# Kernel tuning notes

Hardware: AMD Instinct MI355X
Metric: run time of the kernel (lower is better)

## Reference

```python
import jax, jax.numpy as jnp
import numpy as np

C_A = 768; C_S = 384; C_Z = 128; H = 16; D = C_A // H
B = 1; N = 4096; NQ = 32; NK = 128; NB = N // NQ
EPS = 1e-5


def _ln(x):
    # layernorm without learned affine (affine applied by caller where present)
    m = jnp.mean(x, axis=-1, keepdims=True)
    v = jnp.mean((x - m) ** 2, axis=-1, keepdims=True)
    return (x - m) * jax.lax.rsqrt(v + EPS)


def setup_inputs() -> dict:
    key = jax.random.key(0)
    ks = jax.random.split(key, 16)
    w = lambda k, shp: jax.random.normal(k, shp, dtype=jnp.float32) * 0.02
    return dict(
        a=jax.random.normal(ks[0], (B, N, C_A), jnp.float32),
        s=jax.random.normal(ks[1], (B, N, C_S), jnp.float32),
        z=jax.random.normal(ks[2], (B, NB, NQ, NK, C_Z), jnp.float32),
        adaln_gamma_s=jnp.ones((C_S,), jnp.float32),
        adaln_ws=w(ks[3], (C_S, C_A)),
        adaln_bs=jnp.zeros((C_A,), jnp.float32),
        adaln_wskip=w(ks[4], (C_S, C_A)),
        lnz_gamma=jnp.ones((C_Z,), jnp.float32),
        wz=w(ks[5], (C_Z, H)),
        wq=w(ks[6], (C_A, C_A)), bq=jnp.zeros((C_A,), jnp.float32),
        wk=w(ks[7], (C_A, C_A)),
        wv=w(ks[8], (C_A, C_A)),
        wg=w(ks[9], (C_A, C_A)), bg=jnp.ones((C_A,), jnp.float32),
        wo=w(ks[10], (C_A, C_A)), bo=jnp.zeros((C_A,), jnp.float32),
        w_last=w(ks[11], (C_S, C_A)),
        b_last=jnp.full((C_A,), -2.0, jnp.float32),  # biasinit = -2.0
        n_queries=NQ, n_keys=NK,
    )


def _forward(a, s, z, adaln_gamma_s, adaln_ws, adaln_bs, adaln_wskip,
             lnz_gamma, wz, wq, bq, wk, wv, wg, bg, wo, bo,
             w_last, b_last, n_queries, n_keys):
    Bq, Nq, _ = a.shape
    nb = Nq // n_queries
    # AdaptiveLayerNorm (AF3 Alg 26): a <- sigmoid(Lin(s_ln)) * LN(a) + LinNoBias(s_ln)
    s_ln = _ln(s) * adaln_gamma_s
    a_ln = jax.nn.sigmoid(s_ln @ adaln_ws + adaln_bs) * _ln(a) + s_ln @ adaln_wskip
    # pair bias: LN(z) (no offset) -> per-head bias, permuted to [B,H,nb,nq,nk]
    bias = (_ln(z) * lnz_gamma) @ wz                    # [B, nb, nq, nk, H]
    bias = jnp.transpose(bias, (0, 4, 1, 2, 3))          # [B, H, nb, nq, nk]
    # projections (q has bias; k/v no bias)
    q = (a_ln @ wq + bq).reshape(Bq, nb, n_queries, H, D)
    k = (a_ln @ wk).reshape(Bq, Nq, H, D)
    v = (a_ln @ wv).reshape(Bq, Nq, H, D)
    # local window: query block w covers [w*nq, (w+1)*nq); keys are nk centered on it
    start = jnp.arange(nb) * n_queries + n_queries // 2 - n_keys // 2
    kidx = start[:, None] + jnp.arange(n_keys)[None, :]  # [nb, nk]
    valid = (kidx >= 0) & (kidx < Nq)
    kidx = jnp.clip(kidx, 0, Nq - 1)
    k_loc = k[:, kidx]                                    # [B, nb, nk, H, D]
    v_loc = v[:, kidx]
    scale = 1.0 / float(np.sqrt(D))
    scores = jnp.einsum('bwqhd,bwkhd->bhwqk', q, k_loc) * scale + bias
    scores = jnp.where(valid[None, None, :, None, :], scores, -1e9)
    p = jax.nn.softmax(scores, axis=-1)
    o = jnp.einsum('bhwqk,bwkhd->bwqhd', p, v_loc).reshape(Bq, Nq, C_A)
    # gating, output projection, final sigmoid gate from raw s
    o = (jax.nn.sigmoid(a_ln @ wg + bg) * o) @ wo + bo
    return jax.nn.sigmoid(s @ w_last + b_last) * o


def reference(a, s, z, adaln_gamma_s, adaln_ws, adaln_bs, adaln_wskip,
              lnz_gamma, wz, wq, bq, wk, wv, wg, bg, wo, bo,
              w_last, b_last, n_queries, n_keys):
    return _forward(a, s, z, adaln_gamma_s, adaln_ws, adaln_bs, adaln_wskip,
                    lnz_gamma, wz, wq, bq, wk, wv, wg, bg, wo, bo,
                    w_last, b_last, n_queries, n_keys)
```

## Files before the change

### kernel.cpp

```cpp
#include <hip/hip_runtime.h>
#include <hip/hip_bf16.h>
#include <math.h>

#define N_TOK 4096
#define CA 768
#define CS 384
#define CZ 128
#define NHEAD 16
#define DH 48
#define NQW 32
#define NKW 128
#define NBLK 128
#define VT_W 4224

typedef __attribute__((ext_vector_type(8))) short short8;
typedef __attribute__((ext_vector_type(4))) float float4v;
typedef __attribute__((ext_vector_type(4))) unsigned short ushort4v;

__device__ __forceinline__ float sigmoidf_(float x){ return 1.0f/(1.0f+__expf(-x)); }

__device__ __forceinline__ unsigned short f2bf(float x){
  unsigned u = __float_as_uint(x);
  unsigned r = (u + 0x7FFFu + ((u>>16)&1u)) >> 16;
  return (unsigned short)r;
}
__device__ __forceinline__ float bf2f(unsigned short b){
  return __uint_as_float(((unsigned)b)<<16);
}
__device__ __forceinline__ short8 cvt8(const float* xv){
  union { short8 v; unsigned short u[8]; } H;
  #pragma unroll
  for (int j=0;j<8;j++) H.u[j] = f2bf(xv[j]);
  return H.v;
}

__device__ __forceinline__ void gload_lds16(const void* gsrc, void* ldst){
  __builtin_amdgcn_global_load_lds(
    (const __attribute__((address_space(1))) void*)gsrc,
    (__attribute__((address_space(3))) void*)ldst, 16, 0, 0);
}

__global__ __launch_bounds__(256) void prep_kernel(
  const float* __restrict__ s, const float* __restrict__ adaln_gamma,
  unsigned short* __restrict__ s_ln_h, unsigned short* __restrict__ s_h,
  const float* __restrict__ a, float* __restrict__ a_n,
  const float* __restrict__ ws, const float* __restrict__ wskip,
  const float* __restrict__ wq, const float* __restrict__ wk,
  const float* __restrict__ wv, const float* __restrict__ wg,
  const float* __restrict__ wo, const float* __restrict__ wlast,
  unsigned short* __restrict__ Wt1, unsigned short* __restrict__ Wt2,
  unsigned short* __restrict__ Wt3, unsigned short* __restrict__ Wt4,
  const float* __restrict__ bq, const float* __restrict__ bg,
  float* __restrict__ biasq)
{
  __shared__ float tile[64][65];
  int bid = blockIdx.x;
  int tid = threadIdx.x;

  if (bid < 1024){
    int wave = tid>>6, lane = tid&63;
    int row = bid*4 + wave;
    const float* x = s + (size_t)row*CS;
    float v[6]; float sum=0.f, sq=0.f;
    #pragma unroll
    for (int i=0;i<6;i++){ v[i]=x[lane+64*i]; sum+=v[i]; sq+=v[i]*v[i]; }
    #pragma unroll
    for (int off=32; off; off>>=1){ sum+=__shfl_xor(sum,off); sq+=__shfl_xor(sq,off); }
    float m = sum*(1.f/CS);
    float var = sq*(1.f/CS)-m*m;
    float rs = rsqrtf(var+1e-5f);
    #pragma unroll
    for (int i=0;i<6;i++){
      int c = lane+64*i;
      s_ln_h[(size_t)row*CS+c] = f2bf((v[i]-m)*rs*adaln_gamma[c]);
      s_h[(size_t)row*CS+c]    = f2bf(v[i]);
    }
    return;
  }
  bid -= 1024;

  if (bid < 1024){
    int wave = tid>>6, lane = tid&63;
    int row = bid*4 + wave;
    const float* x = a + (size_t)row*CA;
    float v[12]; float sum=0.f, sq=0.f;
    #pragma unroll
    for (int i=0;i<12;i++){ v[i]=x[lane+64*i]; sum+=v[i]; sq+=v[i]*v[i]; }
    #pragma unroll
    for (int off=32; off; off>>=1){ sum+=__shfl_xor(sum,off); sq+=__shfl_xor(sq,off); }
    float m = sum*(1.f/CA);
    float var = sq*(1.f/CA)-m*m;
    float rs = rsqrtf(var+1e-5f);
    float* o = a_n + (size_t)row*CA;
    #pragma unroll
    for (int i=0;i<12;i++) o[lane+64*i] = (v[i]-m)*rs;
    return;
  }
  bid -= 1024;

  if (bid < 936){
    const float* src; unsigned short* dst; int K; int local;
    if      (bid < 72)  { src=ws;    dst=Wt1;                   K=CS; local=bid; }
    else if (bid < 144) { src=wskip; dst=Wt1 + (size_t)768*CS;  K=CS; local=bid-72; }
    else if (bid < 288) { src=wq;    dst=Wt2;                   K=CA; local=bid-144; }
    else if (bid < 432) { src=wk;    dst=Wt2 + (size_t)768*CA;  K=CA; local=bid-288; }
    else if (bid < 576) { src=wv;    dst=Wt2 + (size_t)1536*CA; K=CA; local=bid-432; }
    else if (bid < 720) { src=wg;    dst=Wt2 + (size_t)2304*CA; K=CA; local=bid-576; }
    else if (bid < 864) { src=wo;    dst=Wt3;                   K=CA; local=bid-720; }
    else                { src=wlast; dst=Wt4;                   K=CS; local=bid-864; }
    int ktiles = K/64;
    int kb = (local % ktiles)*64, nb = (local / ktiles)*64;
    int c = tid & 63, r0 = tid >> 6;
    #pragma unroll
    for (int i=0;i<16;i++){
      int r = r0 + 4*i;
      tile[r][c] = src[(size_t)(kb+r)*CA + nb + c];
    }
    __syncthreads();
    #pragma unroll
    for (int i=0;i<16;i++){
      int r = r0 + 4*i;
      dst[(size_t)(nb+r)*K + kb + c] = f2bf(tile[c][r]);
    }
    return;
  }
  bid -= 936;

  int i = bid*256 + tid;
  float v = 0.f;
  if (i < 768) v = bq[i];
  else if (i >= 2304) v = bg[i-2304];
  biasq[i] = v;
}

__global__ __launch_bounds__(256) void zbias_kernel(const float* __restrict__ z,
                                                    const float* __restrict__ gamma,
                                                    const float* __restrict__ wz,
                                                    unsigned short* __restrict__ bias3){
  __shared__ float tbuf[4][16*132];
  int tid = threadIdx.x, wave = tid>>6, lane = tid&63;
  int lr = lane&15, quad = lane>>4;

  short8 bwh[4];
  float w1 = 0.f;
  #pragma unroll
  for (int ks=0;ks<4;ks++){
    float wv[8];
    #pragma unroll
    for (int j=0;j<8;j++){
      int k = ks*32 + quad*8 + j;
      wv[j] = wz[k*NHEAD + lr]*gamma[k];
      w1 += wv[j];
    }
    bwh[ks] = cvt8(wv);
  }
  w1 += __shfl_xor(w1, 16);
  w1 += __shfl_xor(w1, 32);

  size_t group = (size_t)blockIdx.x*4 + wave;
  const float* zg = z + group*(size_t)(NKW*CZ);

  float4 bufA[8], bufB[8];
  auto loadrow = [&](int b, float4* dst){
    const float* zr = zg + (size_t)(b*16 + lr)*CZ + quad*8;
    #pragma unroll
    for (int ks=0;ks<4;ks++){
      dst[ks*2]   = *(const float4*)(zr + ks*32);
      dst[ks*2+1] = *(const float4*)(zr + ks*32 + 4);
    }
  };
  auto process = [&](int b, const float4* d){
    float sum=0.f, sq=0.f;
    #pragma unroll
    for (int p=0;p<8;p++){
      sum += d[p].x + d[p].y + d[p].z + d[p].w;
      sq  += d[p].x*d[p].x + d[p].y*d[p].y + d[p].z*d[p].z + d[p].w*d[p].w;
    }
    sum += __shfl_xor(sum,16); sum += __shfl_xor(sum,32);
    sq  += __shfl_xor(sq,16);  sq  += __shfl_xor(sq,32);
    float mean = sum*(1.f/CZ);
    float var = sq*(1.f/CZ) - mean*mean;
    float rs = rsqrtf(var + 1e-5f);

    float4v c = (float4v){0.f,0.f,0.f,0.f};
    #pragma unroll
    for (int ks=0;ks<4;ks++){
      float xv[8];
      xv[0]=d[ks*2].x;   xv[1]=d[ks*2].y;   xv[2]=d[ks*2].z;   xv[3]=d[ks*2].w;
      xv[4]=d[ks*2+1].x; xv[5]=d[ks*2+1].y; xv[6]=d[ks*2+1].z; xv[7]=d[ks*2+1].w;
      c = __builtin_amdgcn_mfma_f32_16x16x32_bf16(cvt8(xv), bwh[ks], c, 0,0,0);
    }
    #pragma unroll
    for (int r=0;r<4;r++){
      int rrow = quad*4 + r;
      float m_r  = __shfl(mean, rrow);
      float rs_r = __shfl(rs, rrow);
      tbuf[wave][lr*132 + b*16 + rrow] = rs_r*(c[r] - m_r*w1);
    }
  };

  loadrow(0, bufA);
  #pragma unroll 1
  for (int bb=0;bb<4;bb++){
    loadrow(bb*2+1, bufB);
    process(bb*2, bufA);
    if (bb<3) loadrow(bb*2+2, bufA);
    process(bb*2+1, bufB);
  }

  #pragma unroll
  for (int i=0;i<8;i++){
    int h = i*2 + (lane>>5);
    int koff = (lane&31)*4;
    float4 vv = *(const float4*)&tbuf[wave][h*132 + koff];
    ushort4v o4 = { f2bf(vv.x), f2bf(vv.y), f2bf(vv.z), f2bf(vv.w) };
    *(ushort4v*)(bias3 + group*2048 + h*128 + koff) = o4;
  }
}

__global__ __launch_bounds__(256) void adaln_gemm(
  const unsigned short* __restrict__ A, const unsigned short* __restrict__ Bt,
  const float* __restrict__ bs, const float* __restrict__ a_n,
  unsigned short* __restrict__ outh)
{
  __shared__ unsigned short Ash[128*32];
  __shared__ unsigned short B1sh[128*32];
  __shared__ unsigned short B2sh[128*32];

  int tid = threadIdx.x;
  int w = tid >> 6, lane = tid & 63;
  int lr = lane & 15, quad = lane >> 4;
  int m0 = blockIdx.y*128, n0 = blockIdx.x*128;
  int mbase = (w&1)*64, nbase = (w>>1)*64;

  float4v acc1[4][4], acc2[4][4];
  #pragma unroll
  for (int i=0;i<4;i++)
    #pragma unroll
    for (int j=0;j<4;j++){
      acc1[i][j] = (float4v){0.f,0.f,0.f,0.f};
      acc2[i][j] = (float4v){0.f,0.f,0.f,0.f};
    }

  int grow = w*32 + (lane>>2);
  int gcol8 = (lane&3)*8;

  for (int k0=0; k0<CS; k0+=32){
    __syncthreads();
    #pragma unroll
    for (int i=0;i<2;i++){
      int rA = grow + i*16;
      gload_lds16(A  + (size_t)(m0 + rA)*CS + k0 + gcol8, &Ash[(w*32 + i*16)*32]);
      gload_lds16(Bt + (size_t)(n0 + rA)*CS + k0 + gcol8, &B1sh[(w*32 + i*16)*32]);
      gload_lds16(Bt + (size_t)(768 + n0 + rA)*CS + k0 + gcol8, &B2sh[(w*32 + i*16)*32]);
    }
    __syncthreads();

    short8 af[4], b1f[4], b2f[4];
    #pragma unroll
    for (int mi=0;mi<4;mi++)
      af[mi] = *(const short8*)&Ash[(mbase + mi*16 + lr)*32 + quad*8];
    #pragma unroll
    for (int ni=0;ni<4;ni++){
      b1f[ni] = *(const short8*)&B1sh[(nbase + ni*16 + lr)*32 + quad*8];
      b2f[ni] = *(const short8*)&B2sh[(nbase + ni*16 + lr)*32 + quad*8];
    }
    #pragma unroll
    for (int mi=0;mi<4;mi++)
      #pragma unroll
      for (int ni=0;ni<4;ni++){
        acc1[mi][ni] = __builtin_amdgcn_mfma_f32_16x16x32_bf16(af[mi], b1f[ni], acc1[mi][ni], 0,0,0);
        acc2[mi][ni] = __builtin_amdgcn_mfma_f32_16x16x32_bf16(af[mi], b2f[ni], acc2[mi][ni], 0,0,0);
      }
  }

  #pragma unroll
  for (int ni=0;ni<4;ni++){
    int col = n0 + nbase + ni*16 + lr;
    float bsv = bs[col];
    #pragma unroll
    for (int mi=0;mi<4;mi++){
      #pragma unroll
      for (int reg=0;reg<4;reg++){
        int row = m0 + mbase + mi*16 + quad*4 + reg;
        float v = sigmoidf_(acc1[mi][ni][reg] + bsv)*a_n[(size_t)row*CA + col] + acc2[mi][ni][reg];
        outh[(size_t)row*CA + col] = f2bf(v);
      }
    }
  }
}

template<int MODE>
__global__ __launch_bounds__(256) void gemm_bf16(
  const unsigned short* __restrict__ A1, const unsigned short* __restrict__ B1,
  const float* __restrict__ bias1, int K1,
  const unsigned short* __restrict__ A2, const unsigned short* __restrict__ B2,
  const float* __restrict__ bias2, int K2,
  void* __restrict__ outp, int M, int N)
{
  __shared__ unsigned short Ash[128*32];
  __shared__ unsigned short Bsh[128*32];

  int tid = threadIdx.x;
  int w = tid >> 6, lane = tid & 63;
  int lr = lane & 15, quad = lane >> 4;
  int m0 = blockIdx.y*128, n0 = blockIdx.x*128;
  int mbase = (w&1)*64, nbase = (w>>1)*64;

  float4v acc1[4][4];
  float4v acc2[4][4];
  #pragma unroll
  for (int i=0;i<4;i++)
    #pragma unroll
    for (int j=0;j<4;j++){
      acc1[i][j] = (float4v){0.f,0.f,0.f,0.f};
      if constexpr (MODE == 3) acc2[i][j] = (float4v){0.f,0.f,0.f,0.f};
    }

  int grow = w*32 + (lane>>2);
  int gcol8 = (lane&3)*8;

  for (int k0=0; k0<K1; k0+=32){
    __syncthreads();
    #pragma unroll
    for (int i=0;i<2;i++){
      int rA = grow + i*16;
      gload_lds16(A1 + (size_t)(m0 + rA)*K1 + k0 + gcol8, &Ash[(w*32 + i*16)*32]);
      gload_lds16(B1 + (size_t)(n0 + rA)*K1 + k0 + gcol8, &Bsh[(w*32 + i*16)*32]);
    }
    __syncthreads();

    short8 af[4], bf[4];
    #pragma unroll
    for (int mi=0;mi<4;mi++)
      af[mi] = *(const short8*)&Ash[(mbase + mi*16 + lr)*32 + quad*8];
    #pragma unroll
    for (int ni=0;ni<4;ni++)
      bf[ni] = *(const short8*)&Bsh[(nbase + ni*16 + lr)*32 + quad*8];
    #pragma unroll
    for (int mi=0;mi<4;mi++)
      #pragma unroll
      for (int ni=0;ni<4;ni++)
        acc1[mi][ni] = __builtin_amdgcn_mfma_f32_16x16x32_bf16(af[mi], bf[ni], acc1[mi][ni], 0,0,0);
  }

  if constexpr (MODE == 3){
    for (int k0=0; k0<K2; k0+=32){
      __syncthreads();
      #pragma unroll
      for (int i=0;i<2;i++){
        int rA = grow + i*16;
        gload_lds16(A2 + (size_t)(m0 + rA)*K2 + k0 + gcol8, &Ash[(w*32 + i*16)*32]);
        gload_lds16(B2 + (size_t)(n0 + rA)*K2 + k0 + gcol8, &Bsh[(w*32 + i*16)*32]);
      }
      __syncthreads();

      short8 af[4], bf[4];
      #pragma unroll
      for (int mi=0;mi<4;mi++)
        af[mi] = *(const short8*)&Ash[(mbase + mi*16 + lr)*32 + quad*8];
      #pragma unroll
      for (int ni=0;ni<4;ni++)
        bf[ni] = *(const short8*)&Bsh[(nbase + ni*16 + lr)*32 + quad*8];
      #pragma unroll
      for (int mi=0;mi<4;mi++)
        #pragma unroll
        for (int ni=0;ni<4;ni++)
          acc2[mi][ni] = __builtin_amdgcn_mfma_f32_16x16x32_bf16(af[mi], bf[ni], acc2[mi][ni], 0,0,0);
    }
  }

  #pragma unroll
  for (int ni=0;ni<4;ni++){
    int col = n0 + nbase + ni*16 + lr;
    float bv1 = bias1 ? bias1[col] : 0.f;
    float bv2 = (MODE==3 && bias2) ? bias2[col] : 0.f;
    #pragma unroll
    for (int mi=0;mi<4;mi++){
      #pragma unroll
      for (int reg=0;reg<4;reg++){
        int row = m0 + mbase + mi*16 + quad*4 + reg;
        float x1 = acc1[mi][ni][reg] + bv1;
        if constexpr (MODE == 1)
          ((unsigned short*)outp)[(size_t)row*N + col] = f2bf(x1);
        else
          ((float*)outp)[(size_t)row*N + col] = sigmoidf_(acc2[mi][ni][reg] + bv2)*x1;
      }
    }
  }
}

__global__ __launch_bounds__(256) void vtrans_kernel(const unsigned short* __restrict__ qh,
                                                     unsigned short* __restrict__ Vt){
  __shared__ unsigned short tile[64][66];
  int t0 = blockIdx.x*64, c0 = blockIdx.y*64;
  int tid = threadIdx.x;
  int c = tid & 63, r0 = tid >> 6;
  #pragma unroll
  for (int i=0;i<16;i++){
    int r = r0 + 4*i;
    tile[r][c] = qh[(size_t)(t0+r)*3072 + 1536 + c0 + c];
  }
  if (t0 == 0){
    #pragma unroll
    for (int i=0;i<16;i++){
      int r = r0 + 4*i;
      Vt[(size_t)(c0+r)*VT_W + c] = 0;
    }
  } else if (t0 == N_TOK-64){
    #pragma unroll
    for (int i=0;i<16;i++){
      int r = r0 + 4*i;
      Vt[(size_t)(c0+r)*VT_W + 64 + N_TOK + c] = 0;
    }
  }
  __syncthreads();
  #pragma unroll
  for (int i=0;i<16;i++){
    int r = r0 + 4*i;
    Vt[(size_t)(c0+r)*VT_W + 64 + t0 + c] = tile[c][r];
  }
}

__global__ __launch_bounds__(256) void attn_kernel(
  const unsigned short* __restrict__ qh,
  const unsigned short* __restrict__ Vt,
  const unsigned short* __restrict__ bias3h,
  unsigned short* __restrict__ og)
{
  __shared__ unsigned short Pb[4][32*40];
  int tid = threadIdx.x, wave = tid>>6, lane = tid&63;
  int lr = lane&15, quad = lane>>4;
  int w = blockIdx.x, h = blockIdx.y*4 + wave;
  int start = w*NQW - 48;
  const float scale = 0.14433756729740643f;

  short8 zero8 = {0,0,0,0,0,0,0,0};

  short8 aq[2][2];
  #pragma unroll
  for (int mt=0;mt<2;mt++){
    int row = w*NQW + mt*16 + lr;
    const unsigned short* qp = qh + (size_t)row*3072 + h*DH;
    aq[mt][0] = *(const short8*)(qp + quad*8);
    aq[mt][1] = (quad<2) ? *(const short8*)(qp + 32 + quad*8) : zero8;
  }

  float4v c[2][8];
  #pragma unroll
  for (int mt=0;mt<2;mt++)
    #pragma unroll
    for (int nt=0;nt<8;nt++) c[mt][nt] = (float4v){0.f,0.f,0.f,0.f};

  #pragma unroll 1
  for (int nt=0;nt<8;nt++){
    int krc = min(max(start + nt*16 + lr,0),N_TOK-1);
    const unsigned short* kp = qh + (size_t)krc*3072 + 768 + h*DH;
    short8 bk0 = *(const short8*)(kp + quad*8);
    short8 bk1 = (quad<2) ? *(const short8*)(kp + 32 + quad*8) : zero8;
    #pragma unroll
    for (int mt=0;mt<2;mt++){
      c[mt][nt] = __builtin_amdgcn_mfma_f32_16x16x32_bf16(aq[mt][0], bk0, c[mt][nt], 0,0,0);
      c[mt][nt] = __builtin_amdgcn_mfma_f32_16x16x32_bf16(aq[mt][1], bk1, c[mt][nt], 0,0,0);
    }
  }

  float rmax[2][4], rsum[2][4];
  #pragma unroll
  for (int mt=0;mt<2;mt++)
    #pragma unroll
    for (int r=0;r<4;r++){ rmax[mt][r] = -3.0e38f; rsum[mt][r] = 0.f; }

  #pragma unroll
  for (int nt=0;nt<8;nt++){
    int key = start + nt*16 + lr;
    bool valid = (key>=0) && (key<N_TOK);
    #pragma unroll
    for (int mt=0;mt<2;mt++){
      #pragma unroll
      for (int r=0;r<4;r++){
        int q = mt*16 + quad*4 + r;
        float bv = bf2f(bias3h[(((size_t)(w*NQW+q))*NHEAD + h)*128 + nt*16 + lr]);
        float v = valid ? (c[mt][nt][r]*scale + bv) : -1e9f;
        c[mt][nt][r] = v;
        rmax[mt][r] = fmaxf(rmax[mt][r], v);
      }
    }
  }
  #pragma unroll
  for (int mt=0;mt<2;mt++)
    #pragma unroll
    for (int r=0;r<4;r++){
      float m = rmax[mt][r];
      m = fmaxf(m, __shfl_xor(m,1)); m = fmaxf(m, __shfl_xor(m,2));
      m = fmaxf(m, __shfl_xor(m,4)); m = fmaxf(m, __shfl_xor(m,8));
      rmax[mt][r] = m;
    }
  #pragma unroll
  for (int nt=0;nt<8;nt++)
    #pragma unroll
    for (int mt=0;mt<2;mt++)
      #pragma unroll
      for (int r=0;r<4;r++){
        float e = __expf(c[mt][nt][r] - rmax[mt][r]);
        c[mt][nt][r] = e;
        rsum[mt][r] += e;
      }
  #pragma unroll
  for (int mt=0;mt<2;mt++)
    #pragma unroll
    for (int r=0;r<4;r++){
      float sv = rsum[mt][r];
      sv += __shfl_xor(sv,1); sv += __shfl_xor(sv,2);
      sv += __shfl_xor(sv,4); sv += __shfl_xor(sv,8);
      rsum[mt][r] = 1.f/sv;
    }

  unsigned short* ph = &Pb[wave][0];
  float4v o[2][3];
  #pragma unroll
  for (int mt=0;mt<2;mt++)
    #pragma unroll
    for (int no=0;no<3;no++) o[mt][no] = (float4v){0.f,0.f,0.f,0.f};

  #pragma unroll 1
  for (int c2=0;c2<2;c2++){
    #pragma unroll 1
    for (int ks=0;ks<2;ks++){
      int ntb = c2*4 + ks*2;
      #pragma unroll
      for (int t=0;t<2;t++){
        int nt = ntb + t;
        #pragma unroll
        for (int mt=0;mt<2;mt++){
          #pragma unroll
          for (int r=0;r<4;r++){
            int q = mt*16 + quad*4 + r;
            ph[q*40 + t*16 + lr] = f2bf(c[mt][nt][r]*rsum[mt][r]);
          }
        }
      }
      short8 pa[2];
      #pragma unroll
      for (int mt=0;mt<2;mt++)
        pa[mt] = *(const short8*)&ph[(mt*16+lr)*40 + quad*8];
      #pragma unroll
      for (int no=0;no<3;no++){
        int col = h*DH + no*16 + lr;
        const unsigned short* vp = Vt + (size_t)col*VT_W + 64 + start + c2*64 + ks*32 + quad*8;
        short8 bv = *(const short8*)vp;
        #pragma unroll
        for (int mt=0;mt<2;mt++)
          o[mt][no] = __builtin_amdgcn_mfma_f32_16x16x32_bf16(pa[mt], bv, o[mt][no], 0,0,0);
      }
    }
  }

  #pragma unroll
  for (int mt=0;mt<2;mt++){
    #pragma unroll
    for (int no=0;no<3;no++){
      int d = no*16 + lr;
      #pragma unroll
      for (int r=0;r<4;r++){
        int q = mt*16 + quad*4 + r;
        size_t grow = (size_t)(w*NQW + q);
        float g = bf2f(qh[grow*3072 + 2304 + h*DH + d]);
        og[grow*CA + h*DH + d] = f2bf(o[mt][no][r] * sigmoidf_(g));
      }
    }
  }
}

extern "C" void kernel_launch(void* const* d_in, const int* in_sizes, int n_in,
                              void* d_out, int out_size, void* d_ws, size_t ws_size,
                              hipStream_t stream)
{
  const float* a            = (const float*)d_in[0];
  const float* s            = (const float*)d_in[1];
  const float* z            = (const float*)d_in[2];
  const float* adaln_gamma  = (const float*)d_in[3];
  const float* adaln_ws     = (const float*)d_in[4];
  const float* adaln_bs     = (const float*)d_in[5];
  const float* adaln_wskip  = (const float*)d_in[6];
  const float* lnz_gamma    = (const float*)d_in[7];
  const float* wz           = (const float*)d_in[8];
  const float* wq           = (const float*)d_in[9];
  const float* bq           = (const float*)d_in[10];
  const float* wk           = (const float*)d_in[11];
  const float* wv           = (const float*)d_in[12];
  const float* wg           = (const float*)d_in[13];
  const float* bg           = (const float*)d_in[14];
  const float* wo           = (const float*)d_in[15];
  const float* bo           = (const float*)d_in[16];
  const float* w_last       = (const float*)d_in[17];
  const float* b_last       = (const float*)d_in[18];
  float* out = (float*)d_out;

  char* base = (char*)d_ws;
  size_t off = 0;
  auto alloc = [&](size_t bytes)->char*{ char* p = base + off; off += (bytes + 255) & ~(size_t)255; return p; };

  unsigned short* s_ln_h = (unsigned short*)alloc((size_t)N_TOK*CS*2);
  unsigned short* s_h    = (unsigned short*)alloc((size_t)N_TOK*CS*2);
  float*          a_n    = (float*)alloc((size_t)N_TOK*CA*4);
  unsigned short* a_ln_h = (unsigned short*)alloc((size_t)N_TOK*CA*2);
  unsigned short* og_h   = (unsigned short*)alloc((size_t)N_TOK*CA*2);
  unsigned short* Wt1    = (unsigned short*)alloc((size_t)1536*CS*2);
  unsigned short* Wt2    = (unsigned short*)alloc((size_t)3072*CA*2);
  unsigned short* Wt3    = (unsigned short*)alloc((size_t)CA*CA*2);
  unsigned short* Wt4    = (unsigned short*)alloc((size_t)CA*CS*2);
  unsigned short* bias3h = (unsigned short*)alloc((size_t)N_TOK*NHEAD*NKW*2);
  unsigned short* qkvg_h = (unsigned short*)alloc((size_t)N_TOK*3072*2);
  unsigned short* Vt     = (unsigned short*)alloc((size_t)CA*VT_W*2);
  float*          biasq  = (float*)alloc((size_t)3072*4);

  prep_kernel<<<dim3(1024+1024+936+12), 256, 0, stream>>>(
      s, adaln_gamma, s_ln_h, s_h, a, a_n,
      adaln_ws, adaln_wskip, wq, wk, wv, wg, wo, w_last,
      Wt1, Wt2, Wt3, Wt4, bq, bg, biasq);

  zbias_kernel<<<dim3(N_TOK/4), 256, 0, stream>>>(z, lnz_gamma, wz, bias3h);

  adaln_gemm<<<dim3(CA/128, N_TOK/128), 256, 0, stream>>>(s_ln_h, Wt1, adaln_bs, a_n, a_ln_h);

  gemm_bf16<1><<<dim3(3072/128, N_TOK/128), 256, 0, stream>>>(
      a_ln_h, Wt2, biasq, CA, nullptr, nullptr, nullptr, 0, qkvg_h, N_TOK, 3072);

  vtrans_kernel<<<dim3(N_TOK/64, CA/64), 256, 0, stream>>>(qkvg_h, Vt);

  attn_kernel<<<dim3(NBLK, 4), 256, 0, stream>>>(qkvg_h, Vt, bias3h, og_h);

  gemm_bf16<3><<<dim3(CA/128, N_TOK/128), 256, 0, stream>>>(
      og_h, Wt3, bo, CA, s_h, Wt4, b_last, CS, out, N_TOK, CA);
}
```

Before: 234.8 us.

## Double-buffer GEMM tiles, fuse z-bias into QKVG GEMM launch, prefetch V in attention

All three GEMM kernels now double-buffer their LDS tiles so the global loads for the next K-step are issued before the current step's MFMAs, with one barrier per iteration instead of two. The z-bias layernorm/projection work is merged into the QKVG GEMM launch by interleaving block roles (3 GEMM blocks per 4 z-bias blocks), so the memory-bound z read can overlap compute-bound GEMM tiles. The final GEMM runs both K loops as one pipelined loop. The attention kernel gets launch bounds of 2, partial unrolling of the QK loop, and V fragments prefetched into registers ahead of the softmax, at the cost of more registers and possible spills.

New measurement: 278.0 us. 18.4% more time.

```diff
diff --git a/kernel.cpp b/kernel.cpp
--- a/kernel.cpp
+++ b/kernel.cpp
@@ -133,99 +133,14 @@
   biasq[i] = v;
 }
 
-__global__ __launch_bounds__(256) void zbias_kernel(const float* __restrict__ z,
-                                                    const float* __restrict__ gamma,
-                                                    const float* __restrict__ wz,
-                                                    unsigned short* __restrict__ bias3){
-  __shared__ float tbuf[4][16*132];
-  int tid = threadIdx.x, wave = tid>>6, lane = tid&63;
-  int lr = lane&15, quad = lane>>4;
-
-  short8 bwh[4];
-  float w1 = 0.f;
-  #pragma unroll
-  for (int ks=0;ks<4;ks++){
-    float wv[8];
-    #pragma unroll
-    for (int j=0;j<8;j++){
-      int k = ks*32 + quad*8 + j;
-      wv[j] = wz[k*NHEAD + lr]*gamma[k];
-      w1 += wv[j];
-    }
-    bwh[ks] = cvt8(wv);
-  }
-  w1 += __shfl_xor(w1, 16);
-  w1 += __shfl_xor(w1, 32);
-
-  size_t group = (size_t)blockIdx.x*4 + wave;
-  const float* zg = z + group*(size_t)(NKW*CZ);
-
-  float4 bufA[8], bufB[8];
-  auto loadrow = [&](int b, float4* dst){
-    const float* zr = zg + (size_t)(b*16 + lr)*CZ + quad*8;
-    #pragma unroll
-    for (int ks=0;ks<4;ks++){
-      dst[ks*2]   = *(const float4*)(zr + ks*32);
-      dst[ks*2+1] = *(const float4*)(zr + ks*32 + 4);
-    }
-  };
-  auto process = [&](int b, const float4* d){
-    float sum=0.f, sq=0.f;
-    #pragma unroll
-    for (int p=0;p<8;p++){
-      sum += d[p].x + d[p].y + d[p].z + d[p].w;
-      sq  += d[p].x*d[p].x + d[p].y*d[p].y + d[p].z*d[p].z + d[p].w*d[p].w;
-    }
-    sum += __shfl_xor(sum,16); sum += __shfl_xor(sum,32);
-    sq  += __shfl_xor(sq,16);  sq  += __shfl_xor(sq,32);
-    float mean = sum*(1.f/CZ);
-    float var = sq*(1.f/CZ) - mean*mean;
-    float rs = rsqrtf(var + 1e-5f);
-
-    float4v c = (float4v){0.f,0.f,0.f,0.f};
-    #pragma unroll
-    for (int ks=0;ks<4;ks++){
-      float xv[8];
-      xv[0]=d[ks*2].x;   xv[1]=d[ks*2].y;   xv[2]=d[ks*2].z;   xv[3]=d[ks*2].w;
-      xv[4]=d[ks*2+1].x; xv[5]=d[ks*2+1].y; xv[6]=d[ks*2+1].z; xv[7]=d[ks*2+1].w;
-      c = __builtin_amdgcn_mfma_f32_16x16x32_bf16(cvt8(xv), bwh[ks], c, 0,0,0);
-    }
-    #pragma unroll
-    for (int r=0;r<4;r++){
-      int rrow = quad*4 + r;
-      float m_r  = __shfl(mean, rrow);
-      float rs_r = __shfl(rs, rrow);
-      tbuf[wave][lr*132 + b*16 + rrow] = rs_r*(c[r] - m_r*w1);
-    }
-  };
-
-  loadrow(0, bufA);
-  #pragma unroll 1
-  for (int bb=0;bb<4;bb++){
-    loadrow(bb*2+1, bufB);
-    process(bb*2, bufA);
-    if (bb<3) loadrow(bb*2+2, bufA);
-    process(bb*2+1, bufB);
-  }
-
-  #pragma unroll
-  for (int i=0;i<8;i++){
-    int h = i*2 + (lane>>5);
-    int koff = (lane&31)*4;
-    float4 vv = *(const float4*)&tbuf[wave][h*132 + koff];
-    ushort4v o4 = { f2bf(vv.x), f2bf(vv.y), f2bf(vv.z), f2bf(vv.w) };
-    *(ushort4v*)(bias3 + group*2048 + h*128 + koff) = o4;
-  }
-}
-
 __global__ __launch_bounds__(256) void adaln_gemm(
   const unsigned short* __restrict__ A, const unsigned short* __restrict__ Bt,
   const float* __restrict__ bs, const float* __restrict__ a_n,
   unsigned short* __restrict__ outh)
 {
-  __shared__ unsigned short Ash[128*32];
-  __shared__ unsigned short B1sh[128*32];
-  __shared__ unsigned short B2sh[128*32];
+  __shared__ unsigned short Ash[2][128*32];
+  __shared__ unsigned short B1sh[2][128*32];
+  __shared__ unsigned short B2sh[2][128*32];
 
   int tid = threadIdx.x;
   int w = tid >> 6, lane = tid & 63;
@@ -245,25 +160,31 @@
   int grow = w*32 + (lane>>2);
   int gcol8 = (lane&3)*8;
 
-  for (int k0=0; k0<CS; k0+=32){
-    __syncthreads();
+  auto stage = [&](int buf, int k0){
     #pragma unroll
     for (int i=0;i<2;i++){
       int rA = grow + i*16;
-      gload_lds16(A  + (size_t)(m0 + rA)*CS + k0 + gcol8, &Ash[(w*32 + i*16)*32]);
-      gload_lds16(Bt + (size_t)(n0 + rA)*CS + k0 + gcol8, &B1sh[(w*32 + i*16)*32]);
-      gload_lds16(Bt + (size_t)(768 + n0 + rA)*CS + k0 + gcol8, &B2sh[(w*32 + i*16)*32]);
-    }
-    __syncthreads();
-
+      gload_lds16(A  + (size_t)(m0 + rA)*CS + k0 + gcol8, &Ash[buf][(w*32 + i*16)*32]);
+      gload_lds16(Bt + (size_t)(n0 + rA)*CS + k0 + gcol8, &B1sh[buf][(w*32 + i*16)*32]);
+      gload_lds16(Bt + (size_t)(768 + n0 + rA)*CS + k0 + gcol8, &B2sh[buf][(w*32 + i*16)*32]);
+    }
+  };
+
+  stage(0, 0);
+  __syncthreads();
+  int cur = 0;
+  const int NT = CS/32;
+  #pragma unroll 1
+  for (int t=0; t<NT; ++t){
+    if (t+1 < NT) stage(cur^1, (t+1)*32);
     short8 af[4], b1f[4], b2f[4];
     #pragma unroll
     for (int mi=0;mi<4;mi++)
-      af[mi] = *(const short8*)&Ash[(mbase + mi*16 + lr)*32 + quad*8];
+      af[mi] = *(const short8*)&Ash[cur][(mbase + mi*16 + lr)*32 + quad*8];
     #pragma unroll
     for (int ni=0;ni<4;ni++){
-      b1f[ni] = *(const short8*)&B1sh[(nbase + ni*16 + lr)*32 + quad*8];
-      b2f[ni] = *(const short8*)&B2sh[(nbase + ni*16 + lr)*32 + quad*8];
+      b1f[ni] = *(const short8*)&B1sh[cur][(nbase + ni*16 + lr)*32 + quad*8];
+      b2f[ni] = *(const short8*)&B2sh[cur][(nbase + ni*16 + lr)*32 + quad*8];
     }
     #pragma unroll
     for (int mi=0;mi<4;mi++)
@@ -272,6 +193,7 @@
         acc1[mi][ni] = __builtin_amdgcn_mfma_f32_16x16x32_bf16(af[mi], b1f[ni], acc1[mi][ni], 0,0,0);
         acc2[mi][ni] = __builtin_amdgcn_mfma_f32_16x16x32_bf16(af[mi], b2f[ni], acc2[mi][ni], 0,0,0);
       }
+    if (t+1 < NT){ __syncthreads(); cur ^= 1; }
   }
 
   #pragma unroll
@@ -290,16 +212,173 @@
   }
 }
 
-template<int MODE>
-__global__ __launch_bounds__(256) void gemm_bf16(
+__global__ __launch_bounds__(256) void qkvg_zbias_kernel(
   const unsigned short* __restrict__ A1, const unsigned short* __restrict__ B1,
-  const float* __restrict__ bias1, int K1,
+  const float* __restrict__ biasq, unsigned short* __restrict__ outp,
+  const float* __restrict__ z, const float* __restrict__ gamma,
+  const float* __restrict__ wz, unsigned short* __restrict__ bias3)
+{
+  union SMem {
+    struct { unsigned short A[2][128*32]; unsigned short Bb[2][128*32]; } g;
+    float tb[4][16*132];
+  };
+  __shared__ SMem sm;
+
+  int bid = blockIdx.x;
+  int g7 = bid/7, r7 = bid - g7*7;
+  int tid = threadIdx.x, wave = tid>>6, lane = tid&63;
+  int lr = lane&15, quad = lane>>4;
+
+  if (r7 < 3){
+    int gb = g7*3 + r7;
+    int bx = gb % 24, by = gb / 24;
+    int w = wave;
+    int m0 = by*128, n0 = bx*128;
+    int mbase = (w&1)*64, nbase = (w>>1)*64;
+
+    float4v acc[4][4];
+    #pragma unroll
+    for (int i=0;i<4;i++)
+      #pragma unroll
+      for (int j=0;j<4;j++) acc[i][j] = (float4v){0.f,0.f,0.f,0.f};
+
+    int grow = w*32 + (lane>>2);
+    int gcol8 = (lane&3)*8;
+
+    auto stage = [&](int buf, int k0){
+      #pragma unroll
+      for (int i=0;i<2;i++){
+        int rA = grow + i*16;
+        gload_lds16(A1 + (size_t)(m0 + rA)*CA + k0 + gcol8, &sm.g.A[buf][(w*32 + i*16)*32]);
+        gload_lds16(B1 + (size_t)(n0 + rA)*CA + k0 + gcol8, &sm.g.Bb[buf][(w*32 + i*16)*32]);
+      }
+    };
+
+    stage(0, 0);
+    __syncthreads();
+    int cur = 0;
+    const int NT = CA/32;
+    #pragma unroll 1
+    for (int t=0; t<NT; ++t){
+      if (t+1 < NT) stage(cur^1, (t+1)*32);
+      short8 af[4], bf[4];
+      #pragma unroll
+      for (int mi=0;mi<4;mi++)
+        af[mi] = *(const short8*)&sm.g.A[cur][(mbase + mi*16 + lr)*32 + quad*8];
+      #pragma unroll
+      for (int ni=0;ni<4;ni++)
+        bf[ni] = *(const short8*)&sm.g.Bb[cur][(nbase + ni*16 + lr)*32 + quad*8];
+      #pragma unroll
+      for (int mi=0;mi<4;mi++)
+        #pragma unroll
+        for (int ni=0;ni<4;ni++)
+          acc[mi][ni] = __builtin_amdgcn_mfma_f32_16x16x32_bf16(af[mi], bf[ni], acc[mi][ni], 0,0,0);
+      if (t+1 < NT){ __syncthreads(); cur ^= 1; }
+    }
+
+    #pragma unroll
+    for (int ni=0;ni<4;ni++){
+      int col = n0 + nbase + ni*16 + lr;
+      float bv = biasq[col];
+      #pragma unroll
+      for (int mi=0;mi<4;mi++){
+        #pragma unroll
+        for (int reg=0;reg<4;reg++){
+          int row = m0 + mbase + mi*16 + quad*4 + reg;
+          outp[(size_t)row*3072 + col] = f2bf(acc[mi][ni][reg] + bv);
+        }
+      }
+    }
+  } else {
+    int zb = g7*4 + (r7-3);
+
+    short8 bwh[4];
+    float w1 = 0.f;
+    #pragma unroll
+    for (int ks=0;ks<4;ks++){
+      float wv[8];
+      #pragma unroll
+      for (int j=0;j<8;j++){
+        int k = ks*32 + quad*8 + j;
+        wv[j] = wz[k*NHEAD + lr]*gamma[k];
+        w1 += wv[j];
+      }
+      bwh[ks] = cvt8(wv);
+    }
+    w1 += __shfl_xor(w1, 16);
+    w1 += __shfl_xor(w1, 32);
+
+    size_t group = (size_t)zb*4 + wave;
+    const float* zg = z + group*(size_t)(NKW*CZ);
+
+    float4 bufA[8], bufB[8];
+    auto loadrow = [&](int b, float4* dst){
+      const float* zr = zg + (size_t)(b*16 + lr)*CZ + quad*8;
+      #pragma unroll
+      for (int ks=0;ks<4;ks++){
+        dst[ks*2]   = *(const float4*)(zr + ks*32);
+        dst[ks*2+1] = *(const float4*)(zr + ks*32 + 4);
+      }
+    };
+    auto process = [&](int b, const float4* d){
+      float sum=0.f, sq=0.f;
+      #pragma unroll
+      for (int p=0;p<8;p++){
+        sum += d[p].x + d[p].y + d[p].z + d[p].w;
+        sq  += d[p].x*d[p].x + d[p].y*d[p].y + d[p].z*d[p].z + d[p].w*d[p].w;
+      }
+      sum += __shfl_xor(sum,16); sum += __shfl_xor(sum,32);
+      sq  += __shfl_xor(sq,16);  sq  += __shfl_xor(sq,32);
+      float mean = sum*(1.f/CZ);
+      float var = sq*(1.f/CZ) - mean*mean;
+      float rs = rsqrtf(var + 1e-5f);
+
+      float4v c = (float4v){0.f,0.f,0.f,0.f};
+      #pragma unroll
+      for (int ks=0;ks<4;ks++){
+        float xv[8];
+        xv[0]=d[ks*2].x;   xv[1]=d[ks*2].y;   xv[2]=d[ks*2].z;   xv[3]=d[ks*2].w;
+        xv[4]=d[ks*2+1].x; xv[5]=d[ks*2+1].y; xv[6]=d[ks*2+1].z; xv[7]=d[ks*2+1].w;
+        c = __builtin_amdgcn_mfma_f32_16x16x32_bf16(cvt8(xv), bwh[ks], c, 0,0,0);
+      }
+      #pragma unroll
+      for (int r=0;r<4;r++){
+        int rrow = quad*4 + r;
+        float m_r  = __shfl(mean, rrow);
+        float rs_r = __shfl(rs, rrow);
+        sm.tb[wave][lr*132 + b*16 + rrow] = rs_r*(c[r] - m_r*w1);
+      }
+    };
+
+    loadrow(0, bufA);
+    #pragma unroll 1
+    for (int bb=0;bb<4;bb++){
+      loadrow(bb*2+1, bufB);
+      process(bb*2, bufA);
+      if (bb<3) loadrow(bb*2+2, bufA);
+      process(bb*2+1, bufB);
+    }
+
+    #pragma unroll
+    for (int i=0;i<8;i++){
+      int h = i*2 + (lane>>5);
+      int koff = (lane&31)*4;
+      float4 vv = *(const float4*)&sm.tb[wave][h*132 + koff];
+      ushort4v o4 = { f2bf(vv.x), f2bf(vv.y), f2bf(vv.z), f2bf(vv.w) };
+      *(ushort4v*)(bias3 + group*2048 + h*128 + koff) = o4;
+    }
+  }
+}
+
+__global__ __launch_bounds__(256) void gemm_final(
+  const unsigned short* __restrict__ A1, const unsigned short* __restrict__ B1,
+  const float* __restrict__ bias1,
   const unsigned short* __restrict__ A2, const unsigned short* __restrict__ B2,
-  const float* __restrict__ bias2, int K2,
-  void* __restrict__ outp, int M, int N)
+  const float* __restrict__ bias2,
+  float* __restrict__ outp)
 {
-  __shared__ unsigned short Ash[128*32];
-  __shared__ unsigned short Bsh[128*32];
+  __shared__ unsigned short Ash[2][128*32];
+  __shared__ unsigned short Bsh[2][128*32];
 
   int tid = threadIdx.x;
   int w = tid >> 6, lane = tid & 63;
@@ -307,84 +386,72 @@
   int m0 = blockIdx.y*128, n0 = blockIdx.x*128;
   int mbase = (w&1)*64, nbase = (w>>1)*64;
 
-  float4v acc1[4][4];
-  float4v acc2[4][4];
+  float4v acc1[4][4], acc2[4][4];
   #pragma unroll
   for (int i=0;i<4;i++)
     #pragma unroll
     for (int j=0;j<4;j++){
       acc1[i][j] = (float4v){0.f,0.f,0.f,0.f};
-      if constexpr (MODE == 3) acc2[i][j] = (float4v){0.f,0.f,0.f,0.f};
+      acc2[i][j] = (float4v){0.f,0.f,0.f,0.f};
     }
 
   int grow = w*32 + (lane>>2);
   int gcol8 = (lane&3)*8;
 
-  for (int k0=0; k0<K1; k0+=32){
-    __syncthreads();
+  const int NT1 = CA/32, NT2 = CS/32, NT = NT1+NT2;
+
+  auto stage = [&](int buf, int t){
+    const unsigned short* Ap; const unsigned short* Bp; int K, k0;
+    if (t < NT1){ Ap=A1; Bp=B1; K=CA; k0=t*32; }
+    else        { Ap=A2; Bp=B2; K=CS; k0=(t-NT1)*32; }
     #pragma unroll
     for (int i=0;i<2;i++){
       int rA = grow + i*16;
-      gload_lds16(A1 + (size_t)(m0 + rA)*K1 + k0 + gcol8, &Ash[(w*32 + i*16)*32]);
-      gload_lds16(B1 + (size_t)(n0 + rA)*K1 + k0 + gcol8, &Bsh[(w*32 + i*16)*32]);
-    }
-    __syncthreads();
-
+      gload_lds16(Ap + (size_t)(m0 + rA)*K + k0 + gcol8, &Ash[buf][(w*32 + i*16)*32]);
+      gload_lds16(Bp + (size_t)(n0 + rA)*K + k0 + gcol8, &Bsh[buf][(w*32 + i*16)*32]);
+    }
+  };
+
+  stage(0, 0);
+  __syncthreads();
+  int cur = 0;
+  #pragma unroll 1
+  for (int t=0; t<NT; ++t){
+    if (t+1 < NT) stage(cur^1, t+1);
     short8 af[4], bf[4];
     #pragma unroll
     for (int mi=0;mi<4;mi++)
-      af[mi] = *(const short8*)&Ash[(mbase + mi*16 + lr)*32 + quad*8];
+      af[mi] = *(const short8*)&Ash[cur][(mbase + mi*16 + lr)*32 + quad*8];
     #pragma unroll
     for (int ni=0;ni<4;ni++)
-      bf[ni] = *(const short8*)&Bsh[(nbase + ni*16 + lr)*32 + quad*8];
-    #pragma unroll
-    for (int mi=0;mi<4;mi++)
-      #pragma unroll
-      for (int ni=0;ni<4;ni++)
-        acc1[mi][ni] = __builtin_amdgcn_mfma_f32_16x16x32_bf16(af[mi], bf[ni], acc1[mi][ni], 0,0,0);
-  }
-
-  if constexpr (MODE == 3){
-    for (int k0=0; k0<K2; k0+=32){
-      __syncthreads();
-      #pragma unroll
-      for (int i=0;i<2;i++){
-        int rA = grow + i*16;
-        gload_lds16(A2 + (size_t)(m0 + rA)*K2 + k0 + gcol8, &Ash[(w*32 + i*16)*32]);
-        gload_lds16(B2 + (size_t)(n0 + rA)*K2 + k0 + gcol8, &Bsh[(w*32 + i*16)*32]);
-      }
-      __syncthreads();
-
-      short8 af[4], bf[4];
+      bf[ni] = *(const short8*)&Bsh[cur][(nbase + ni*16 + lr)*32 + quad*8];
+    if (t < NT1){
       #pragma unroll
       for (int mi=0;mi<4;mi++)
-        af[mi] = *(const short8*)&Ash[(mbase + mi*16 + lr)*32 + quad*8];
-      #pragma unroll
-      for (int ni=0;ni<4;ni++)
-        bf[ni] = *(const short8*)&Bsh[(nbase + ni*16 + lr)*32 + quad*8];
+        #pragma unroll
+        for (int ni=0;ni<4;ni++)
+          acc1[mi][ni] = __builtin_amdgcn_mfma_f32_16x16x32_bf16(af[mi], bf[ni], acc1[mi][ni], 0,0,0);
+    } else {
       #pragma unroll
       for (int mi=0;mi<4;mi++)
         #pragma unroll
         for (int ni=0;ni<4;ni++)
           acc2[mi][ni] = __builtin_amdgcn_mfma_f32_16x16x32_bf16(af[mi], bf[ni], acc2[mi][ni], 0,0,0);
     }
+    if (t+1 < NT){ __syncthreads(); cur ^= 1; }
   }
 
   #pragma unroll
   for (int ni=0;ni<4;ni++){
     int col = n0 + nbase + ni*16 + lr;
-    float bv1 = bias1 ? bias1[col] : 0.f;
-    float bv2 = (MODE==3 && bias2) ? bias2[col] : 0.f;
+    float bv1 = bias1[col];
+    float bv2 = bias2[col];
     #pragma unroll
     for (int mi=0;mi<4;mi++){
       #pragma unroll
       for (int reg=0;reg<4;reg++){
         int row = m0 + mbase + mi*16 + quad*4 + reg;
-        float x1 = acc1[mi][ni][reg] + bv1;
-        if constexpr (MODE == 1)
-          ((unsigned short*)outp)[(size_t)row*N + col] = f2bf(x1);
-        else
-          ((float*)outp)[(size_t)row*N + col] = sigmoidf_(acc2[mi][ni][reg] + bv2)*x1;
+        outp[(size_t)row*CA + col] = sigmoidf_(acc2[mi][ni][reg] + bv2)*(acc1[mi][ni][reg] + bv1);
       }
     }
   }
@@ -422,7 +489,7 @@
   }
 }
 
-__global__ __launch_bounds__(256) void attn_kernel(
+__global__ __launch_bounds__(256,2) void attn_kernel(
   const unsigned short* __restrict__ qh,
   const unsigned short* __restrict__ Vt,
   const unsigned short* __restrict__ bias3h,
@@ -452,7 +519,7 @@
     #pragma unroll
     for (int nt=0;nt<8;nt++) c[mt][nt] = (float4v){0.f,0.f,0.f,0.f};
 
-  #pragma unroll 1
+  #pragma unroll 2
   for (int nt=0;nt<8;nt++){
     int krc = min(max(start + nt*16 + lr,0),N_TOK-1);
     const unsigned short* kp = qh + (size_t)krc*3072 + 768 + h*DH;
@@ -464,6 +531,17 @@
       c[mt][nt] = __builtin_amdgcn_mfma_f32_16x16x32_bf16(aq[mt][1], bk1, c[mt][nt], 0,0,0);
     }
   }
+
+  short8 vb[2][2][3];
+  #pragma unroll
+  for (int c2=0;c2<2;c2++)
+    #pragma unroll
+    for (int ks=0;ks<2;ks++)
+      #pragma unroll
+      for (int no=0;no<3;no++){
+        int col = h*DH + no*16 + lr;
+        vb[c2][ks][no] = *(const short8*)(Vt + (size_t)col*VT_W + 64 + start + c2*64 + ks*32 + quad*8);
+      }
 
   float rmax[2][4], rsum[2][4];
   #pragma unroll
@@ -523,9 +601,9 @@
     #pragma unroll
     for (int no=0;no<3;no++) o[mt][no] = (float4v){0.f,0.f,0.f,0.f};
 
-  #pragma unroll 1
+  #pragma unroll
   for (int c2=0;c2<2;c2++){
-    #pragma unroll 1
+    #pragma unroll
     for (int ks=0;ks<2;ks++){
       int ntb = c2*4 + ks*2;
       #pragma unroll
@@ -546,12 +624,9 @@
         pa[mt] = *(const short8*)&ph[(mt*16+lr)*40 + quad*8];
       #pragma unroll
       for (int no=0;no<3;no++){
-        int col = h*DH + no*16 + lr;
-        const unsigned short* vp = Vt + (size_t)col*VT_W + 64 + start + c2*64 + ks*32 + quad*8;
-        short8 bv = *(const short8*)vp;
         #pragma unroll
         for (int mt=0;mt<2;mt++)
-          o[mt][no] = __builtin_amdgcn_mfma_f32_16x16x32_bf16(pa[mt], bv, o[mt][no], 0,0,0);
+          o[mt][no] = __builtin_amdgcn_mfma_f32_16x16x32_bf16(pa[mt], vb[c2][ks][no], o[mt][no], 0,0,0);
       }
     }
   }
@@ -620,17 +695,15 @@
       adaln_ws, adaln_wskip, wq, wk, wv, wg, wo, w_last,
       Wt1, Wt2, Wt3, Wt4, bq, bg, biasq);
 
-  zbias_kernel<<<dim3(N_TOK/4), 256, 0, stream>>>(z, lnz_gamma, wz, bias3h);
-
   adaln_gemm<<<dim3(CA/128, N_TOK/128), 256, 0, stream>>>(s_ln_h, Wt1, adaln_bs, a_n, a_ln_h);
 
-  gemm_bf16<1><<<dim3(3072/128, N_TOK/128), 256, 0, stream>>>(
-      a_ln_h, Wt2, biasq, CA, nullptr, nullptr, nullptr, 0, qkvg_h, N_TOK, 3072);
+  qkvg_zbias_kernel<<<dim3(1792), 256, 0, stream>>>(
+      a_ln_h, Wt2, biasq, qkvg_h, z, lnz_gamma, wz, bias3h);
 
   vtrans_kernel<<<dim3(N_TOK/64, CA/64), 256, 0, stream>>>(qkvg_h, Vt);
 
   attn_kernel<<<dim3(NBLK, 4), 256, 0, stream>>>(qkvg_h, Vt, bias3h, og_h);
 
-  gemm_bf16<3><<<dim3(CA/128, N_TOK/128), 256, 0, stream>>>(
-      og_h, Wt3, bo, CA, s_h, Wt4, b_last, CS, out, N_TOK, CA);
-}
+  gemm_final<<<dim3(CA/128, N_TOK/128), 256, 0, stream>>>(
+      og_h, Wt3, bo, s_h, Wt4, b_last, out);
+}
```
